# Performance work log

Hardware: AMD Instinct MI355X
Metric: run time of the kernel (lower is better)

Reference implementation:

```python
import jax, jax.numpy as jnp
import numpy as np

D_MODEL = 1024
N_HEADS = 16
HEAD_DIM = D_MODEL // N_HEADS
WINDOW = 256


def setup_inputs() -> dict:
    key = jax.random.key(0)
    kx, kq, ko = jax.random.split(key, 3)
    B, T = 4, 2048
    x = jax.random.normal(kx, (B, T, D_MODEL), dtype=jnp.float32)
    s = 1.0 / np.sqrt(D_MODEL)
    w_qkv = jax.random.normal(kq, (D_MODEL, 3 * D_MODEL), dtype=jnp.float32) * s
    w_out = jax.random.normal(ko, (D_MODEL, D_MODEL), dtype=jnp.float32) * s
    return {"x": x, "w_qkv": w_qkv, "w_out": w_out}


def reference(x, w_qkv, w_out):
    B, T, C = x.shape
    qkv = (x @ w_qkv).reshape(B, T, 3, N_HEADS, HEAD_DIM)
    q, k, v = qkv[:, :, 0], qkv[:, :, 1], qkv[:, :, 2]  # [B,T,H,D]
    # sliding-window causal mask: position i attends to j in (i-W, i]
    i = jnp.arange(T)[:, None]
    j = jnp.arange(T)[None, :]
    allowed = (j <= i) & (j > i - WINDOW)
    mask = jnp.where(allowed, 0.0, -jnp.inf).astype(x.dtype)  # [T,T]
    scale = 1.0 / np.sqrt(HEAD_DIM)
    scores = jnp.einsum('bqhd,bkhd->bhqk', q, k) * scale + mask
    attn = jax.nn.softmax(scores, axis=-1)
    out = jnp.einsum('bhqk,bkhd->bqhd', attn, v).reshape(B, T, C)
    return out @ w_out
```

## Files before the change

### kernel.cpp

```cpp
#include <hip/hip_runtime.h>

typedef unsigned short u16;
typedef __attribute__((ext_vector_type(8))) short bh8;
typedef __attribute__((ext_vector_type(4))) float f4;
typedef __attribute__((ext_vector_type(4))) unsigned short us4;

#define T_SEQ 2048
#define NHEADS 16
#define DHEAD 64
#define WIN 256

__device__ __forceinline__ float bf2f(u16 u) {
  union { unsigned int i; float f; } v; v.i = ((unsigned int)u) << 16; return v.f;
}
__device__ __forceinline__ u16 f2bf(float f) {
  unsigned int u = __float_as_uint(f);
  u = u + 0x7fffu + ((u >> 16) & 1u);
  return (u16)(u >> 16);
}
__device__ __forceinline__ void async16(const void* g, void* l) {
  void* gv = const_cast<void*>(g);
  __builtin_amdgcn_global_load_lds(
      (__attribute__((address_space(1))) void*)gv,
      (__attribute__((address_space(3))) void*)l, 16, 0, 0);
}

__device__ __forceinline__ int is_f32_probe(const void* x) {
  const float* xf = (const float*)x;
  const int lane = threadIdx.x & 63;
  int bad = 0;
  #pragma unroll
  for (int u = 0; u < 4; ++u) {
    const float v = xf[lane * 4 + u];
    const float a = fabsf(v);
    bad |= (!(a < 64.f)) || (!(v == 0.f || a > 1e-30f));
  }
  return __any(bad) ? 0 : 1;
}

__global__ __launch_bounds__(256) void prep(
    const void* __restrict__ x, const void* __restrict__ w_qkv,
    const void* __restrict__ w_out, u16* __restrict__ xbf,
    u16* __restrict__ wqkvT, u16* __restrict__ woutT, int have_x)
{
  const int bid = blockIdx.x;
  const int tid = threadIdx.x;
  const int isf = is_f32_probe(x);

  if (bid < 4096) {
    if (!have_x) return;
    const size_t e = ((size_t)bid * 256 + tid) * 8;
    if (isf) {
      const float* f = (const float*)x;
      us4 o0, o1;
      #pragma unroll
      for (int u = 0; u < 4; ++u) { o0[u] = f2bf(f[e + u]); o1[u] = f2bf(f[e + 4 + u]); }
      *(us4*)&xbf[e] = o0; *(us4*)&xbf[e + 4] = o1;
    } else {
      *(us4*)&xbf[e]     = *(const us4*)&((const u16*)x)[e];
      *(us4*)&xbf[e + 4] = *(const us4*)&((const u16*)x)[e + 4];
    }
  } else {
    __shared__ alignas(16) u16 tile[32][33];
    const void* in; u16* out; int C, bx, by;
    if (bid < 4096 + 3072) { const int t = bid - 4096; in = w_qkv; out = wqkvT; C = 3072; bx = t % 96; by = t / 96; }
    else                   { const int t = bid - 7168; in = w_out; out = woutT; C = 1024; bx = t % 32; by = t / 32; }
    const int R = 1024;
    const int tx = tid & 31, ty = tid >> 5;
    const int xg = bx * 32 + tx;
    const int y0 = by * 32;
    #pragma unroll
    for (int i = ty; i < 32; i += 8) {
      u16 v;
      if (isf) v = f2bf(((const float*)in)[(size_t)(y0 + i) * C + xg]);
      else     v = ((const u16*)in)[(size_t)(y0 + i) * C + xg];
      tile[i][tx] = v;
    }
    __syncthreads();
    const int ox  = y0 + tx;
    const int oy0 = bx * 32;
    #pragma unroll
    for (int i = ty; i < 32; i += 8)
      out[(size_t)(oy0 + i) * R + ox] = tile[tx][i];
  }
}

template<bool ADYN, bool CDYN>
__global__ __launch_bounds__(256, 4) void gemm_bt(
    const void* __restrict__ A, const u16* __restrict__ Bt,
    void* __restrict__ C, int N, int K, int lda, int ldc,
    const void* __restrict__ xprobe)
{
  __shared__ alignas(16) u16 As[128 * 64];
  __shared__ alignas(16) u16 Bs[128 * 64];

  const int isf  = (ADYN || CDYN) ? is_f32_probe(xprobe) : 0;
  const int tid  = threadIdx.x;
  const int lane = tid & 63;
  const int w    = tid >> 6;
  const int wm   = (w >> 1) * 64;
  const int wn   = (w & 1) * 64;
  const int quad = lane >> 4;
  const int l16  = lane & 15;
  const int row0 = blockIdx.y * 128;
  const int col0 = blockIdx.x * 128;

  f4 acc[4][4] = {};

  size_t aoff[4]; const u16* bsrc[4]; int lofs[4];
  #pragma unroll
  for (int s = 0; s < 4; ++s) {
    const int r  = s * 32 + (tid >> 3);
    const int gc = (tid & 7) ^ (r & 7);
    aoff[s] = (size_t)(row0 + r) * lda + gc * 8;
    bsrc[s] = Bt + (size_t)(col0 + r) * K + gc * 8;
    lofs[s] = s * 4096 + tid * 16;
  }

  const bool af32 = ADYN && isf;

  for (int k0 = 0; k0 < K; k0 += 64) {
    if (af32) {
      const float* Af = (const float*)A;
      bh8 a[4];
      #pragma unroll
      for (int s = 0; s < 4; ++s) {
        f4 u0 = *(const f4*)(Af + aoff[s] + k0);
        f4 u1 = *(const f4*)(Af + aoff[s] + k0 + 4);
        #pragma unroll
        for (int u = 0; u < 4; ++u) { a[s][u] = (short)f2bf(u0[u]); a[s][u + 4] = (short)f2bf(u1[u]); }
      }
      __syncthreads();
      #pragma unroll
      for (int s = 0; s < 4; ++s) {
        *(bh8*)((char*)As + lofs[s]) = a[s];
        async16(bsrc[s] + k0, (char*)Bs + lofs[s]);
      }
    } else {
      const u16* A16 = (const u16*)A;
      __syncthreads();
      #pragma unroll
      for (int s = 0; s < 4; ++s) {
        async16(A16 + aoff[s] + k0, (char*)As + lofs[s]);
        async16(bsrc[s] + k0,       (char*)Bs + lofs[s]);
      }
    }
    __builtin_amdgcn_s_waitcnt(0);
    __syncthreads();

    #pragma unroll
    for (int ks = 0; ks < 2; ++ks) {
      bh8 af[4], bf[4];
      #pragma unroll
      for (int i = 0; i < 4; ++i) {
        const int row = wm + i * 16 + l16;
        const int lc  = (ks * 4 + quad) ^ (row & 7);
        af[i] = *(const bh8*)(As + row * 64 + lc * 8);
      }
      #pragma unroll
      for (int j = 0; j < 4; ++j) {
        const int row = wn + j * 16 + l16;
        const int lc  = (ks * 4 + quad) ^ (row & 7);
        bf[j] = *(const bh8*)(Bs + row * 64 + lc * 8);
      }
      #pragma unroll
      for (int i = 0; i < 4; ++i)
        #pragma unroll
        for (int j = 0; j < 4; ++j)
          acc[i][j] = __builtin_amdgcn_mfma_f32_16x16x32_bf16(af[i], bf[j], acc[i][j], 0, 0, 0);
    }
  }

  const bool cf32 = CDYN && isf;
  #pragma unroll
  for (int i = 0; i < 4; ++i) {
    #pragma unroll
    for (int j = 0; j < 4; ++j) {
      const int rb = row0 + wm + i * 16 + quad * 4;
      const int cc = col0 + wn + j * 16 + l16;
      #pragma unroll
      for (int r = 0; r < 4; ++r) {
        if (cf32) ((float*)C)[(size_t)(rb + r) * ldc + cc] = acc[i][j][r];
        else      ((u16*)C)[(size_t)(rb + r) * ldc + cc]   = f2bf(acc[i][j][r]);
      }
    }
  }
}

__global__ __launch_bounds__(256) void attn_mfma(const u16* __restrict__ qkv,
                                                 u16* __restrict__ att, int ldo)
{
  __shared__ alignas(16) u16 Kt[64 * 72];
  __shared__ alignas(16) u16 Vt[64 * 72];
  __shared__ alignas(16) u16 Ps[64 * 72];

  const int tid  = threadIdx.x;
  const int lane = tid & 63;
  const int w    = tid >> 6;
  const int quad = lane >> 4;
  const int l16  = lane & 15;
  const int qb = blockIdx.x, h = blockIdx.y, b = blockIdx.z;
  const int qs = qb * 64;

  const u16* base = qkv + (size_t)b * T_SEQ * 3072 + h * 64;

  const size_t qrowg = (size_t)(qs + w * 16 + l16) * 3072;
  bh8 qa0 = *(const bh8*)&base[qrowg + quad * 8];
  bh8 qa1 = *(const bh8*)&base[qrowg + 32 + quad * 8];
  #pragma unroll
  for (int u = 0; u < 8; ++u) {
    qa0[u] = (short)f2bf(bf2f((u16)qa0[u]) * 0.125f);
    qa1[u] = (short)f2bf(bf2f((u16)qa1[u]) * 0.125f);
  }

  f4 Oc[4] = {};
  float mst[4] = {-1e30f, -1e30f, -1e30f, -1e30f};
  float lst[4] = {0.f, 0.f, 0.f, 0.f};

  const int tmin = (qb >= 4) ? 0 : (4 - qb);
  const int c8  = (tid & 7) * 8;
  const int r0s = tid >> 3;

  for (int t = tmin; t < 5; ++t) {
    const int kt0 = qs - 256 + t * 64;
    const bool diag  = (t == 4);
    const bool ledge = (t == 0);
    const int kb_lo = ledge ? w : 0;
    const int kb_hi = diag  ? w : 3;
    __syncthreads();

    #pragma unroll
    for (int r = r0s; r < 64; r += 32) {
      *(bh8*)&Kt[r * 72 + c8] =
          *(const bh8*)&base[(size_t)(kt0 + r) * 3072 + 1024 + c8];
      bh8 v = *(const bh8*)&base[(size_t)(kt0 + r) * 3072 + 2048 + c8];
      const int kc = r >> 3, ki = r & 7;
      #pragma unroll
      for (int u = 0; u < 8; ++u) {
        const int d = c8 + u;
        Vt[d * 72 + ((kc ^ (d >> 3)) << 3) + ki] = (u16)v[u];
      }
    }
    __syncthreads();

    f4 S[4];
    #pragma unroll
    for (int kb = 0; kb < 4; ++kb) {
      if (kb < kb_lo || kb > kb_hi) {
        S[kb][0] = S[kb][1] = S[kb][2] = S[kb][3] = -1e30f;
      } else {
        const int krow = (kb * 16 + l16) * 72;
        bh8 kf0 = *(const bh8*)&Kt[krow + quad * 8];
        bh8 kf1 = *(const bh8*)&Kt[krow + 32 + quad * 8];
        f4 s = {};
        s = __builtin_amdgcn_mfma_f32_16x16x32_bf16(qa0, kf0, s, 0, 0, 0);
        s = __builtin_amdgcn_mfma_f32_16x16x32_bf16(qa1, kf1, s, 0, 0, 0);
        S[kb] = s;
      }
    }

    if (diag || ledge) {
      #pragma unroll
      for (int kb = 0; kb < 4; ++kb) {
        if (kb == w) {
          #pragma unroll
          for (int rr = 0; rr < 4; ++rr) {
            const int ii = quad * 4 + rr;
            const bool ok = diag ? (l16 <= ii) : (l16 > ii);
            if (!ok) S[kb][rr] = -1e30f;
          }
        }
      }
    }

    float tmax[4] = {-1e30f, -1e30f, -1e30f, -1e30f};
    #pragma unroll
    for (int kb = 0; kb < 4; ++kb)
      #pragma unroll
      for (int rr = 0; rr < 4; ++rr)
        tmax[rr] = fmaxf(tmax[rr], S[kb][rr]);
    #pragma unroll
    for (int off = 1; off < 16; off <<= 1)
      #pragma unroll
      for (int rr = 0; rr < 4; ++rr)
        tmax[rr] = fmaxf(tmax[rr], __shfl_xor(tmax[rr], off));

    const bool grew = (tmax[0] > mst[0] + 8.f) || (tmax[1] > mst[1] + 8.f) ||
                      (tmax[2] > mst[2] + 8.f) || (tmax[3] > mst[3] + 8.f);
    if (__any(grew)) {
      #pragma unroll
      for (int rr = 0; rr < 4; ++rr) {
        const float mnew = fmaxf(mst[rr], tmax[rr]);
        const float al = __expf(mst[rr] - mnew);
        mst[rr] = mnew;
        lst[rr] *= al;
        #pragma unroll
        for (int db = 0; db < 4; ++db) Oc[db][rr] *= al;
      }
    }

    float rsum[4] = {0.f, 0.f, 0.f, 0.f};
    const int swq = quad >> 1;
    #pragma unroll
    for (int kb = 0; kb < 4; ++kb) {
      const int kc = kb * 2 + (l16 >> 3);
      const int ki = l16 & 7;
      #pragma unroll
      for (int rr = 0; rr < 4; ++rr) {
        const float p = __expf(S[kb][rr] - mst[rr]);
        rsum[rr] += p;
        const int q = w * 16 + quad * 4 + rr;
        Ps[q * 72 + ((kc ^ swq) << 3) + ki] = f2bf(p);
      }
    }
    #pragma unroll
    for (int off = 1; off < 16; off <<= 1)
      #pragma unroll
      for (int rr = 0; rr < 4; ++rr)
        rsum[rr] += __shfl_xor(rsum[rr], off);
    #pragma unroll
    for (int rr = 0; rr < 4; ++rr)
      lst[rr] += rsum[rr];

    {
      const int q = w * 16 + l16;
      const int sw = (q >> 3) & 1;
      bh8 pa0 = *(const bh8*)&Ps[q * 72 + (((0 + quad) ^ sw) << 3)];
      bh8 pa1 = *(const bh8*)&Ps[q * 72 + (((4 + quad) ^ sw) << 3)];
      #pragma unroll
      for (int db = 0; db < 4; ++db) {
        const int d = db * 16 + l16;
        const int dsw = d >> 3;
        bh8 vb0 = *(const bh8*)&Vt[d * 72 + (((0 + quad) ^ dsw) << 3)];
        bh8 vb1 = *(const bh8*)&Vt[d * 72 + (((4 + quad) ^ dsw) << 3)];
        Oc[db] = __builtin_amdgcn_mfma_f32_16x16x32_bf16(pa0, vb0, Oc[db], 0, 0, 0);
        Oc[db] = __builtin_amdgcn_mfma_f32_16x16x32_bf16(pa1, vb1, Oc[db], 0, 0, 0);
      }
    }
  }

  u16* obase = att + (size_t)b * T_SEQ * ldo + h * 64;
  #pragma unroll
  for (int rr = 0; rr < 4; ++rr) {
    const int i = qs + w * 16 + quad * 4 + rr;
    const float inv = 1.f / lst[rr];
    #pragma unroll
    for (int db = 0; db < 4; ++db)
      obase[(size_t)i * ldo + db * 16 + l16] = f2bf(Oc[db][rr] * inv);
  }
}

extern "C" void kernel_launch(void* const* d_in, const int* in_sizes, int n_in,
                              void* d_out, int out_size, void* d_ws, size_t ws_size,
                              hipStream_t stream) {
  const void* x     = d_in[0];
  const void* w_qkv = d_in[1];
  const void* w_out = d_in[2];

  const size_t SZ_QKV = (size_t)8192 * 3072 * 2;
  const size_t SZ_XBF = (size_t)8192 * 1024 * 2;
  const size_t SZ_WQ  = (size_t)3072 * 1024 * 2;
  const size_t SZ_WO  = (size_t)1024 * 1024 * 2;
  const size_t SZ_ATT = (size_t)8192 * 1024 * 2;

  char* p = (char*)d_ws;
  u16* qkv   = (u16*)p; p += SZ_QKV;
  u16* wqkvT = (u16*)p; p += SZ_WQ;
  u16* woutT = (u16*)p; p += SZ_WO;
  u16* xbf   = (u16*)p; p += SZ_XBF;
  u16* attb  = (u16*)p;
  const size_t need_x   = SZ_QKV + SZ_WQ + SZ_WO + SZ_XBF;
  const bool have_x   = ws_size >= need_x;
  const bool have_att = ws_size >= need_x + SZ_ATT;

  prep<<<dim3(8192), 256, 0, stream>>>(x, w_qkv, w_out, xbf, wqkvT, woutT,
                                       have_x ? 1 : 0);

  if (have_x) {
    gemm_bt<false, false><<<dim3(24, 64), 256, 0, stream>>>(
        xbf, wqkvT, qkv, 3072, 1024, 1024, 3072, x);
  } else {
    gemm_bt<true, false><<<dim3(24, 64), 256, 0, stream>>>(
        x, wqkvT, qkv, 3072, 1024, 1024, 3072, x);
  }

  u16* attp  = have_att ? attb : qkv;
  const int ldo = have_att ? 1024 : 3072;
  attn_mfma<<<dim3(32, NHEADS, 4), 256, 0, stream>>>(qkv, attp, ldo);

  gemm_bt<false, true><<<dim3(8, 64), 256, 0, stream>>>(
      attp, woutT, d_out, 1024, 1024, ldo, 1024, x);
}
```

Before: 226.6 us.

## Add double-buffered 256x128 GEMM and pre-transposed V attention path

Adds a new 512-thread GEMM kernel with 256x128 tiles, double-buffered async global-to-LDS loads, split B-fragment phases and s_setprio around the MFMA bursts. It is used for both the QKV and output projections. Adds a separate V-transpose kernel so the attention kernel can fill K and V into swizzled LDS with async loads instead of per-element scattered transposes. This removes load latency and LDS scatter cost, but adds one extra kernel launch and an extra round trip of V through memory, and it needs more workspace.

After: 234.6 us. 1.04x slower.

```diff
diff --git a/kernel.cpp b/kernel.cpp
--- a/kernel.cpp
+++ b/kernel.cpp
@@ -9,6 +9,9 @@
 #define NHEADS 16
 #define DHEAD 64
 #define WIN 256
+
+#define MF(a, b, c) __builtin_amdgcn_mfma_f32_16x16x32_bf16((a), (b), (c), 0, 0, 0)
+#define VMCNT(n) asm volatile("s_waitcnt vmcnt(" #n ")" ::: "memory")
 
 __device__ __forceinline__ float bf2f(u16 u) {
   union { unsigned int i; float f; } v; v.i = ((unsigned int)u) << 16; return v.f;
@@ -167,7 +170,7 @@
       for (int i = 0; i < 4; ++i)
         #pragma unroll
         for (int j = 0; j < 4; ++j)
-          acc[i][j] = __builtin_amdgcn_mfma_f32_16x16x32_bf16(af[i], bf[j], acc[i][j], 0, 0, 0);
+          acc[i][j] = MF(af[i], bf[j], acc[i][j]);
     }
   }
 
@@ -187,11 +190,155 @@
   }
 }
 
-__global__ __launch_bounds__(256) void attn_mfma(const u16* __restrict__ qkv,
-                                                 u16* __restrict__ att, int ldo)
+template<bool CDYN>
+__global__ __launch_bounds__(512, 2) void gemm2(
+    const u16* __restrict__ A, const u16* __restrict__ Bt, void* __restrict__ C,
+    int K, int lda, int ldc, const void* __restrict__ xprobe)
 {
-  __shared__ alignas(16) u16 Kt[64 * 72];
-  __shared__ alignas(16) u16 Vt[64 * 72];
+  __shared__ alignas(16) u16 As[2 * 256 * 64];
+  __shared__ alignas(16) u16 Bs[2 * 128 * 64];
+
+  const int isf  = CDYN ? is_f32_probe(xprobe) : 0;
+  const int tid  = threadIdx.x;
+  const int lane = tid & 63;
+  const int w    = tid >> 6;
+  const int wm   = (w >> 1) * 64;
+  const int wn   = (w & 1) * 64;
+  const int quad = lane >> 4;
+  const int l16  = lane & 15;
+  const int row0 = blockIdx.y * 256;
+  const int col0 = blockIdx.x * 128;
+
+  f4 acc[4][4] = {};
+
+  const int rs = tid >> 3;
+  const int cs = tid & 7;
+  const u16* apt[4]; const u16* bpt[2];
+  #pragma unroll
+  for (int s = 0; s < 4; ++s) {
+    const int r = s * 64 + rs;
+    apt[s] = A + (size_t)(row0 + r) * lda + (cs ^ (r & 7)) * 8;
+  }
+  #pragma unroll
+  for (int s = 0; s < 2; ++s) {
+    const int r = s * 64 + rs;
+    bpt[s] = Bt + (size_t)(col0 + r) * K + (cs ^ (r & 7)) * 8;
+  }
+  const int soff = tid * 16;
+  const int NK = K >> 6;
+
+#define STAGE_A2(buf, kk) do { \
+    async16(apt[0] + (kk), (char*)As + (buf) * 32768 +     0 + soff); \
+    async16(apt[1] + (kk), (char*)As + (buf) * 32768 +  8192 + soff); \
+    async16(apt[2] + (kk), (char*)As + (buf) * 32768 + 16384 + soff); \
+    async16(apt[3] + (kk), (char*)As + (buf) * 32768 + 24576 + soff); } while (0)
+#define STAGE_B2(buf, kk) do { \
+    async16(bpt[0] + (kk), (char*)Bs + (buf) * 16384 +     0 + soff); \
+    async16(bpt[1] + (kk), (char*)Bs + (buf) * 16384 +  8192 + soff); } while (0)
+
+  const int sw = l16 & 7;
+  const int c0 = (quad ^ sw) * 8;
+  const int c1 = ((quad + 4) ^ sw) * 8;
+  int ra[4], rb[4];
+  #pragma unroll
+  for (int i = 0; i < 4; ++i) ra[i] = (wm + i * 16 + l16) * 64;
+  #pragma unroll
+  for (int j = 0; j < 4; ++j) rb[j] = (wn + j * 16 + l16) * 64;
+
+  STAGE_A2(0, 0); STAGE_B2(0, 0);
+  if (NK > 1) { STAGE_A2(1, 64); STAGE_B2(1, 64); VMCNT(6); }
+  else        { VMCNT(0); }
+  __builtin_amdgcn_s_barrier();
+
+  for (int T = 0; T < NK; ++T) {
+    const u16* Ab = As + (T & 1) * 16384;
+    const u16* Bb = Bs + (T & 1) * 8192;
+
+    bh8 a[4][2], b0[2][2];
+    #pragma unroll
+    for (int i = 0; i < 4; ++i) {
+      a[i][0] = *(const bh8*)(Ab + ra[i] + c0);
+      a[i][1] = *(const bh8*)(Ab + ra[i] + c1);
+    }
+    #pragma unroll
+    for (int j = 0; j < 2; ++j) {
+      b0[j][0] = *(const bh8*)(Bb + rb[j] + c0);
+      b0[j][1] = *(const bh8*)(Bb + rb[j] + c1);
+    }
+    if (T >= 1 && T + 1 < NK) STAGE_B2((T + 1) & 1, (T + 1) * 64);
+    __builtin_amdgcn_s_barrier();
+    __builtin_amdgcn_s_setprio(1);
+    #pragma unroll
+    for (int i = 0; i < 4; ++i)
+      #pragma unroll
+      for (int j = 0; j < 2; ++j)
+        acc[i][j] = MF(a[i][1], b0[j][1], MF(a[i][0], b0[j][0], acc[i][j]));
+    __builtin_amdgcn_s_setprio(0);
+    __builtin_amdgcn_s_barrier();
+
+    bh8 b1[2][2];
+    #pragma unroll
+    for (int j = 0; j < 2; ++j) {
+      b1[j][0] = *(const bh8*)(Bb + rb[2 + j] + c0);
+      b1[j][1] = *(const bh8*)(Bb + rb[2 + j] + c1);
+    }
+    if (T + 2 < NK) STAGE_A2(T & 1, (T + 2) * 64);
+    __builtin_amdgcn_s_barrier();
+    __builtin_amdgcn_s_setprio(1);
+    #pragma unroll
+    for (int i = 0; i < 4; ++i)
+      #pragma unroll
+      for (int j = 0; j < 2; ++j)
+        acc[i][2 + j] = MF(a[i][1], b1[j][1], MF(a[i][0], b1[j][0], acc[i][2 + j]));
+    __builtin_amdgcn_s_setprio(0);
+    if (T + 2 < NK) { VMCNT(4); } else { VMCNT(0); }
+    __builtin_amdgcn_s_barrier();
+  }
+#undef STAGE_A2
+#undef STAGE_B2
+
+  const bool cf32 = CDYN && isf;
+  #pragma unroll
+  for (int i = 0; i < 4; ++i) {
+    #pragma unroll
+    for (int j = 0; j < 4; ++j) {
+      const int rr0 = row0 + wm + i * 16 + quad * 4;
+      const int cc  = col0 + wn + j * 16 + l16;
+      #pragma unroll
+      for (int r = 0; r < 4; ++r) {
+        if (cf32) ((float*)C)[(size_t)(rr0 + r) * ldc + cc] = acc[i][j][r];
+        else      ((u16*)C)[(size_t)(rr0 + r) * ldc + cc]   = f2bf(acc[i][j][r]);
+      }
+    }
+  }
+}
+
+__global__ __launch_bounds__(256) void vtrans(const u16* __restrict__ qkv,
+                                              u16* __restrict__ vT)
+{
+  __shared__ alignas(16) u16 tile[32][33];
+  const int tid = threadIdx.x;
+  const int bh = blockIdx.z;
+  const int b = bh >> 4, h = bh & 15;
+  const int k0 = blockIdx.x * 32, d0 = blockIdx.y * 32;
+  const int tx = tid & 31, ty = tid >> 5;
+  const u16* src = qkv + (size_t)b * T_SEQ * 3072 + 2048 + h * 64;
+  #pragma unroll
+  for (int i = ty; i < 32; i += 8)
+    tile[i][tx] = src[(size_t)(k0 + i) * 3072 + d0 + tx];
+  __syncthreads();
+  u16* dst = vT + ((size_t)bh * 64 + d0) * T_SEQ + k0;
+  #pragma unroll
+  for (int i = ty; i < 32; i += 8)
+    dst[(size_t)i * T_SEQ + tx] = tile[tx][i];
+}
+
+__global__ __launch_bounds__(256) void attn_mfma2(const u16* __restrict__ qkv,
+                                                  const u16* __restrict__ vT,
+                                                  u16* __restrict__ att, int ldo)
+{
+  __shared__ alignas(16) u16 Kt[64 * 64];
+  __shared__ alignas(16) u16 Vt[64 * 64];
   __shared__ alignas(16) u16 Ps[64 * 72];
 
   const int tid  = threadIdx.x;
@@ -203,6 +350,7 @@
   const int qs = qb * 64;
 
   const u16* base = qkv + (size_t)b * T_SEQ * 3072 + h * 64;
+  const u16* vTbh = vT + (size_t)(b * NHEADS + h) * 64 * T_SEQ;
 
   const size_t qrowg = (size_t)(qs + w * 16 + l16) * 3072;
   bh8 qa0 = *(const bh8*)&base[qrowg + quad * 8];
@@ -218,8 +366,10 @@
   float lst[4] = {0.f, 0.f, 0.f, 0.f};
 
   const int tmin = (qb >= 4) ? 0 : (4 - qb);
-  const int c8  = (tid & 7) * 8;
-  const int r0s = tid >> 3;
+  const int srow0 = tid >> 3;
+  const int srow1 = 32 + (tid >> 3);
+  const int gc0 = (tid & 7) ^ (srow0 & 7);
+  const int gc1 = (tid & 7) ^ (srow1 & 7);
 
   for (int t = tmin; t < 5; ++t) {
     const int kt0 = qs - 256 + t * 64;
@@ -227,37 +377,32 @@
     const bool ledge = (t == 0);
     const int kb_lo = ledge ? w : 0;
     const int kb_hi = diag  ? w : 3;
+
     __syncthreads();
-
-    #pragma unroll
-    for (int r = r0s; r < 64; r += 32) {
-      *(bh8*)&Kt[r * 72 + c8] =
-          *(const bh8*)&base[(size_t)(kt0 + r) * 3072 + 1024 + c8];
-      bh8 v = *(const bh8*)&base[(size_t)(kt0 + r) * 3072 + 2048 + c8];
-      const int kc = r >> 3, ki = r & 7;
-      #pragma unroll
-      for (int u = 0; u < 8; ++u) {
-        const int d = c8 + u;
-        Vt[d * 72 + ((kc ^ (d >> 3)) << 3) + ki] = (u16)v[u];
-      }
-    }
+    async16(&base[(size_t)(kt0 + srow0) * 3072 + 1024 + gc0 * 8], (char*)Kt + tid * 16);
+    async16(&base[(size_t)(kt0 + srow1) * 3072 + 1024 + gc1 * 8], (char*)Kt + 4096 + tid * 16);
+    async16(vTbh + (size_t)srow0 * T_SEQ + kt0 + gc0 * 8, (char*)Vt + tid * 16);
+    async16(vTbh + (size_t)srow1 * T_SEQ + kt0 + gc1 * 8, (char*)Vt + 4096 + tid * 16);
+    __builtin_amdgcn_s_waitcnt(0);
     __syncthreads();
 
     f4 S[4];
+    __builtin_amdgcn_s_setprio(1);
     #pragma unroll
     for (int kb = 0; kb < 4; ++kb) {
       if (kb < kb_lo || kb > kb_hi) {
         S[kb][0] = S[kb][1] = S[kb][2] = S[kb][3] = -1e30f;
       } else {
-        const int krow = (kb * 16 + l16) * 72;
-        bh8 kf0 = *(const bh8*)&Kt[krow + quad * 8];
-        bh8 kf1 = *(const bh8*)&Kt[krow + 32 + quad * 8];
+        const int row = kb * 16 + l16;
+        bh8 kf0 = *(const bh8*)&Kt[row * 64 + ((quad    ) ^ (row & 7)) * 8];
+        bh8 kf1 = *(const bh8*)&Kt[row * 64 + ((quad + 4) ^ (row & 7)) * 8];
         f4 s = {};
-        s = __builtin_amdgcn_mfma_f32_16x16x32_bf16(qa0, kf0, s, 0, 0, 0);
-        s = __builtin_amdgcn_mfma_f32_16x16x32_bf16(qa1, kf1, s, 0, 0, 0);
+        s = MF(qa0, kf0, s);
+        s = MF(qa1, kf1, s);
         S[kb] = s;
       }
     }
+    __builtin_amdgcn_s_setprio(0);
 
     if (diag || ledge) {
       #pragma unroll
@@ -324,17 +469,181 @@
 
     {
       const int q = w * 16 + l16;
-      const int sw = (q >> 3) & 1;
-      bh8 pa0 = *(const bh8*)&Ps[q * 72 + (((0 + quad) ^ sw) << 3)];
-      bh8 pa1 = *(const bh8*)&Ps[q * 72 + (((4 + quad) ^ sw) << 3)];
+      const int swp = (q >> 3) & 1;
+      bh8 pa0 = *(const bh8*)&Ps[q * 72 + (((0 + quad) ^ swp) << 3)];
+      bh8 pa1 = *(const bh8*)&Ps[q * 72 + (((4 + quad) ^ swp) << 3)];
+      __builtin_amdgcn_s_setprio(1);
+      #pragma unroll
+      for (int db = 0; db < 4; ++db) {
+        const int d = db * 16 + l16;
+        bh8 vb0 = *(const bh8*)&Vt[d * 64 + ((quad    ) ^ (d & 7)) * 8];
+        bh8 vb1 = *(const bh8*)&Vt[d * 64 + ((quad + 4) ^ (d & 7)) * 8];
+        Oc[db] = MF(pa0, vb0, Oc[db]);
+        Oc[db] = MF(pa1, vb1, Oc[db]);
+      }
+      __builtin_amdgcn_s_setprio(0);
+    }
+  }
+
+  u16* obase = att + (size_t)b * T_SEQ * ldo + h * 64;
+  #pragma unroll
+  for (int rr = 0; rr < 4; ++rr) {
+    const int i = qs + w * 16 + quad * 4 + rr;
+    const float inv = 1.f / lst[rr];
+    #pragma unroll
+    for (int db = 0; db < 4; ++db)
+      obase[(size_t)i * ldo + db * 16 + l16] = f2bf(Oc[db][rr] * inv);
+  }
+}
+
+__global__ __launch_bounds__(256) void attn_mfma(const u16* __restrict__ qkv,
+                                                 u16* __restrict__ att, int ldo)
+{
+  __shared__ alignas(16) u16 Kt[64 * 72];
+  __shared__ alignas(16) u16 Vt[64 * 72];
+  __shared__ alignas(16) u16 Ps[64 * 72];
+
+  const int tid  = threadIdx.x;
+  const int lane = tid & 63;
+  const int w    = tid >> 6;
+  const int quad = lane >> 4;
+  const int l16  = lane & 15;
+  const int qb = blockIdx.x, h = blockIdx.y, b = blockIdx.z;
+  const int qs = qb * 64;
+
+  const u16* base = qkv + (size_t)b * T_SEQ * 3072 + h * 64;
+
+  const size_t qrowg = (size_t)(qs + w * 16 + l16) * 3072;
+  bh8 qa0 = *(const bh8*)&base[qrowg + quad * 8];
+  bh8 qa1 = *(const bh8*)&base[qrowg + 32 + quad * 8];
+  #pragma unroll
+  for (int u = 0; u < 8; ++u) {
+    qa0[u] = (short)f2bf(bf2f((u16)qa0[u]) * 0.125f);
+    qa1[u] = (short)f2bf(bf2f((u16)qa1[u]) * 0.125f);
+  }
+
+  f4 Oc[4] = {};
+  float mst[4] = {-1e30f, -1e30f, -1e30f, -1e30f};
+  float lst[4] = {0.f, 0.f, 0.f, 0.f};
+
+  const int tmin = (qb >= 4) ? 0 : (4 - qb);
+  const int c8  = (tid & 7) * 8;
+  const int r0s = tid >> 3;
+
+  for (int t = tmin; t < 5; ++t) {
+    const int kt0 = qs - 256 + t * 64;
+    const bool diag  = (t == 4);
+    const bool ledge = (t == 0);
+    const int kb_lo = ledge ? w : 0;
+    const int kb_hi = diag  ? w : 3;
+    __syncthreads();
+
+    #pragma unroll
+    for (int r = r0s; r < 64; r += 32) {
+      *(bh8*)&Kt[r * 72 + c8] =
+          *(const bh8*)&base[(size_t)(kt0 + r) * 3072 + 1024 + c8];
+      bh8 v = *(const bh8*)&base[(size_t)(kt0 + r) * 3072 + 2048 + c8];
+      const int kc = r >> 3, ki = r & 7;
+      #pragma unroll
+      for (int u = 0; u < 8; ++u) {
+        const int d = c8 + u;
+        Vt[d * 72 + ((kc ^ (d >> 3)) << 3) + ki] = (u16)v[u];
+      }
+    }
+    __syncthreads();
+
+    f4 S[4];
+    #pragma unroll
+    for (int kb = 0; kb < 4; ++kb) {
+      if (kb < kb_lo || kb > kb_hi) {
+        S[kb][0] = S[kb][1] = S[kb][2] = S[kb][3] = -1e30f;
+      } else {
+        const int krow = (kb * 16 + l16) * 72;
+        bh8 kf0 = *(const bh8*)&Kt[krow + quad * 8];
+        bh8 kf1 = *(const bh8*)&Kt[krow + 32 + quad * 8];
+        f4 s = {};
+        s = MF(qa0, kf0, s);
+        s = MF(qa1, kf1, s);
+        S[kb] = s;
+      }
+    }
+
+    if (diag || ledge) {
+      #pragma unroll
+      for (int kb = 0; kb < 4; ++kb) {
+        if (kb == w) {
+          #pragma unroll
+          for (int rr = 0; rr < 4; ++rr) {
+            const int ii = quad * 4 + rr;
+            const bool ok = diag ? (l16 <= ii) : (l16 > ii);
+            if (!ok) S[kb][rr] = -1e30f;
+          }
+        }
+      }
+    }
+
+    float tmax[4] = {-1e30f, -1e30f, -1e30f, -1e30f};
+    #pragma unroll
+    for (int kb = 0; kb < 4; ++kb)
+      #pragma unroll
+      for (int rr = 0; rr < 4; ++rr)
+        tmax[rr] = fmaxf(tmax[rr], S[kb][rr]);
+    #pragma unroll
+    for (int off = 1; off < 16; off <<= 1)
+      #pragma unroll
+      for (int rr = 0; rr < 4; ++rr)
+        tmax[rr] = fmaxf(tmax[rr], __shfl_xor(tmax[rr], off));
+
+    const bool grew = (tmax[0] > mst[0] + 8.f) || (tmax[1] > mst[1] + 8.f) ||
+                      (tmax[2] > mst[2] + 8.f) || (tmax[3] > mst[3] + 8.f);
+    if (__any(grew)) {
+      #pragma unroll
+      for (int rr = 0; rr < 4; ++rr) {
+        const float mnew = fmaxf(mst[rr], tmax[rr]);
+        const float al = __expf(mst[rr] - mnew);
+        mst[rr] = mnew;
+        lst[rr] *= al;
+        #pragma unroll
+        for (int db = 0; db < 4; ++db) Oc[db][rr] *= al;
+      }
+    }
+
+    float rsum[4] = {0.f, 0.f, 0.f, 0.f};
+    const int swq = quad >> 1;
+    #pragma unroll
+    for (int kb = 0; kb < 4; ++kb) {
+      const int kc = kb * 2 + (l16 >> 3);
+      const int ki = l16 & 7;
+      #pragma unroll
+      for (int rr = 0; rr < 4; ++rr) {
+        const float p = __expf(S[kb][rr] - mst[rr]);
+        rsum[rr] += p;
+        const int q = w * 16 + quad * 4 + rr;
+        Ps[q * 72 + ((kc ^ swq) << 3) + ki] = f2bf(p);
+      }
+    }
+    #pragma unroll
+    for (int off = 1; off < 16; off <<= 1)
+      #pragma unroll
+      for (int rr = 0; rr < 4; ++rr)
+        rsum[rr] += __shfl_xor(rsum[rr], off);
+    #pragma unroll
+    for (int rr = 0; rr < 4; ++rr)
+      lst[rr] += rsum[rr];
+
+    {
+      const int q = w * 16 + l16;
+      const int swp = (q >> 3) & 1;
+      bh8 pa0 = *(const bh8*)&Ps[q * 72 + (((0 + quad) ^ swp) << 3)];
+      bh8 pa1 = *(const bh8*)&Ps[q * 72 + (((4 + quad) ^ swp) << 3)];
       #pragma unroll
       for (int db = 0; db < 4; ++db) {
         const int d = db * 16 + l16;
         const int dsw = d >> 3;
         bh8 vb0 = *(const bh8*)&Vt[d * 72 + (((0 + quad) ^ dsw) << 3)];
         bh8 vb1 = *(const bh8*)&Vt[d * 72 + (((4 + quad) ^ dsw) << 3)];
-        Oc[db] = __builtin_amdgcn_mfma_f32_16x16x32_bf16(pa0, vb0, Oc[db], 0, 0, 0);
-        Oc[db] = __builtin_amdgcn_mfma_f32_16x16x32_bf16(pa1, vb1, Oc[db], 0, 0, 0);
+        Oc[db] = MF(pa0, vb0, Oc[db]);
+        Oc[db] = MF(pa1, vb1, Oc[db]);
       }
     }
   }
@@ -361,6 +670,7 @@
   const size_t SZ_XBF = (size_t)8192 * 1024 * 2;
   const size_t SZ_WQ  = (size_t)3072 * 1024 * 2;
   const size_t SZ_WO  = (size_t)1024 * 1024 * 2;
+  const size_t SZ_VT  = (size_t)64 * 64 * 2048 * 2;
   const size_t SZ_ATT = (size_t)8192 * 1024 * 2;
 
   char* p = (char*)d_ws;
@@ -368,26 +678,38 @@
   u16* wqkvT = (u16*)p; p += SZ_WQ;
   u16* woutT = (u16*)p; p += SZ_WO;
   u16* xbf   = (u16*)p; p += SZ_XBF;
+  u16* vTb   = (u16*)p; p += SZ_VT;
   u16* attb  = (u16*)p;
-  const size_t need_x   = SZ_QKV + SZ_WQ + SZ_WO + SZ_XBF;
-  const bool have_x   = ws_size >= need_x;
-  const bool have_att = ws_size >= need_x + SZ_ATT;
+  const size_t need_x  = SZ_QKV + SZ_WQ + SZ_WO + SZ_XBF;
+  const bool have_x    = ws_size >= need_x;
+  const bool have_vt   = ws_size >= need_x + SZ_VT;
+  const bool have_att  = ws_size >= need_x + SZ_VT + SZ_ATT;
 
   prep<<<dim3(8192), 256, 0, stream>>>(x, w_qkv, w_out, xbf, wqkvT, woutT,
                                        have_x ? 1 : 0);
 
   if (have_x) {
-    gemm_bt<false, false><<<dim3(24, 64), 256, 0, stream>>>(
-        xbf, wqkvT, qkv, 3072, 1024, 1024, 3072, x);
+    gemm2<false><<<dim3(24, 32), 512, 0, stream>>>(
+        xbf, wqkvT, qkv, 1024, 1024, 3072, x);
   } else {
     gemm_bt<true, false><<<dim3(24, 64), 256, 0, stream>>>(
         x, wqkvT, qkv, 3072, 1024, 1024, 3072, x);
   }
 
-  u16* attp  = have_att ? attb : qkv;
+  u16* attp = have_att ? attb : qkv;
   const int ldo = have_att ? 1024 : 3072;
-  attn_mfma<<<dim3(32, NHEADS, 4), 256, 0, stream>>>(qkv, attp, ldo);
-
-  gemm_bt<false, true><<<dim3(8, 64), 256, 0, stream>>>(
-      attp, woutT, d_out, 1024, 1024, ldo, 1024, x);
-}
+  if (have_vt) {
+    vtrans<<<dim3(64, 2, 64), 256, 0, stream>>>(qkv, vTb);
+    attn_mfma2<<<dim3(32, NHEADS, 4), 256, 0, stream>>>(qkv, vTb, attp, ldo);
+  } else {
+    attn_mfma<<<dim3(32, NHEADS, 4), 256, 0, stream>>>(qkv, attp, ldo);
+  }
+
+  if (have_x) {
+    gemm2<true><<<dim3(8, 32), 512, 0, stream>>>(
+        attp, woutT, d_out, 1024, ldo, 1024, x);
+  } else {
+    gemm_bt<false, true><<<dim3(8, 64), 256, 0, stream>>>(
+        attp, woutT, d_out, 1024, 1024, ldo, 1024, x);
+  }
+}
```

## Rewrite windowed attention as single-pass block with full K/V window in LDS

Applied to the files above, without the earlier changes.

The attention kernel now processes 128 query rows per 512-thread block and loads the whole 384-row K/V window into LDS once, K through async global-to-LDS copies. Scores for all 17 key tiles stay in registers, and softmax runs without max subtraction or online rescaling. This removes the per-tile sync loop and repeated K/V reloads. Separately, the GEMM gets an XCD-aware block swizzle and the weight transpose in prep is vectorised. Skipping the max subtraction risks exp overflow if scores get large, and the larger LDS footprint and register use may lower occupancy.

Measured after the change: 224.5 us. About the same (-0.9%).

```diff
diff --git a/kernel.cpp b/kernel.cpp
--- a/kernel.cpp
+++ b/kernel.cpp
@@ -4,11 +4,14 @@
 typedef __attribute__((ext_vector_type(8))) short bh8;
 typedef __attribute__((ext_vector_type(4))) float f4;
 typedef __attribute__((ext_vector_type(4))) unsigned short us4;
+typedef __attribute__((ext_vector_type(8))) unsigned short us8;
 
 #define T_SEQ 2048
 #define NHEADS 16
 #define DHEAD 64
 #define WIN 256
+
+#define MF(a, b, c) __builtin_amdgcn_mfma_f32_16x16x32_bf16((a), (b), (c), 0, 0, 0)
 
 __device__ __forceinline__ float bf2f(u16 u) {
   union { unsigned int i; float f; } v; v.i = ((unsigned int)u) << 16; return v.f;
@@ -66,22 +69,24 @@
     if (bid < 4096 + 3072) { const int t = bid - 4096; in = w_qkv; out = wqkvT; C = 3072; bx = t % 96; by = t / 96; }
     else                   { const int t = bid - 7168; in = w_out; out = woutT; C = 1024; bx = t % 32; by = t / 32; }
     const int R = 1024;
-    const int tx = tid & 31, ty = tid >> 5;
-    const int xg = bx * 32 + tx;
+    const int tx4 = (tid & 7) * 4;
+    const int iy  = tid >> 3;
     const int y0 = by * 32;
-    #pragma unroll
-    for (int i = ty; i < 32; i += 8) {
-      u16 v;
-      if (isf) v = f2bf(((const float*)in)[(size_t)(y0 + i) * C + xg]);
-      else     v = ((const u16*)in)[(size_t)(y0 + i) * C + xg];
-      tile[i][tx] = v;
+    if (isf) {
+      f4 v = *(const f4*)&((const float*)in)[(size_t)(y0 + iy) * C + bx * 32 + tx4];
+      #pragma unroll
+      for (int u = 0; u < 4; ++u) tile[iy][tx4 + u] = f2bf(v[u]);
+    } else {
+      us4 v = *(const us4*)&((const u16*)in)[(size_t)(y0 + iy) * C + bx * 32 + tx4];
+      #pragma unroll
+      for (int u = 0; u < 4; ++u) tile[iy][tx4 + u] = v[u];
     }
     __syncthreads();
-    const int ox  = y0 + tx;
-    const int oy0 = bx * 32;
-    #pragma unroll
-    for (int i = ty; i < 32; i += 8)
-      out[(size_t)(oy0 + i) * R + ox] = tile[tx][i];
+    const int i2 = tid >> 3;
+    us4 o;
+    #pragma unroll
+    for (int u = 0; u < 4; ++u) o[u] = tile[tx4 + u][i2];
+    *(us4*)&out[(size_t)(bx * 32 + i2) * R + y0 + tx4] = o;
   }
 }
 
@@ -102,8 +107,18 @@
   const int wn   = (w & 1) * 64;
   const int quad = lane >> 4;
   const int l16  = lane & 15;
-  const int row0 = blockIdx.y * 128;
-  const int col0 = blockIdx.x * 128;
+
+  int bx = blockIdx.x, by = blockIdx.y;
+  {
+    const int nx = gridDim.x, nwg = nx * gridDim.y;
+    if ((nwg & 7) == 0) {
+      const int lin = by * nx + bx;
+      const int sw  = (lin & 7) * (nwg >> 3) + (lin >> 3);
+      bx = sw % nx; by = sw / nx;
+    }
+  }
+  const int row0 = by * 128;
+  const int col0 = bx * 128;
 
   f4 acc[4][4] = {};
 
@@ -167,7 +182,7 @@
       for (int i = 0; i < 4; ++i)
         #pragma unroll
         for (int j = 0; j < 4; ++j)
-          acc[i][j] = __builtin_amdgcn_mfma_f32_16x16x32_bf16(af[i], bf[j], acc[i][j], 0, 0, 0);
+          acc[i][j] = MF(af[i], bf[j], acc[i][j]);
     }
   }
 
@@ -187,12 +202,12 @@
   }
 }
 
-__global__ __launch_bounds__(256) void attn_mfma(const u16* __restrict__ qkv,
-                                                 u16* __restrict__ att, int ldo)
+__global__ __launch_bounds__(512) void attn_win(const u16* __restrict__ qkv,
+                                                u16* __restrict__ att, int ldo)
 {
-  __shared__ alignas(16) u16 Kt[64 * 72];
-  __shared__ alignas(16) u16 Vt[64 * 72];
-  __shared__ alignas(16) u16 Ps[64 * 72];
+  __shared__ alignas(16) u16 Kt[384 * 64];
+  __shared__ alignas(16) u16 Vt[64 * 384];
+  __shared__ alignas(16) u16 Ps[8 * 16 * 72];
 
   const int tid  = threadIdx.x;
   const int lane = tid & 63;
@@ -200,11 +215,36 @@
   const int quad = lane >> 4;
   const int l16  = lane & 15;
   const int qb = blockIdx.x, h = blockIdx.y, b = blockIdx.z;
-  const int qs = qb * 64;
+  const int qs = qb * 128;
+  const int kbase = qs - 256;
 
   const u16* base = qkv + (size_t)b * T_SEQ * 3072 + h * 64;
 
-  const size_t qrowg = (size_t)(qs + w * 16 + l16) * 3072;
+  #pragma unroll
+  for (int s = 0; s < 6; ++s) {
+    const int id = s * 512 + tid;
+    const int r  = id >> 3;
+    const int gc = (id & 7) ^ (r & 7);
+    int gk = kbase + r; gk = gk < 0 ? 0 : gk;
+    async16(&base[(size_t)gk * 3072 + 1024 + gc * 8], (char*)Kt + id * 16);
+  }
+  #pragma unroll
+  for (int s = 0; s < 6; ++s) {
+    const int id = s * 512 + tid;
+    const int r  = id >> 3;
+    const int dc = id & 7;
+    int gk = kbase + r; gk = gk < 0 ? 0 : gk;
+    us8 v = *(const us8*)&base[(size_t)gk * 3072 + 2048 + dc * 8];
+    const int g = r >> 3, j = r & 7;
+    #pragma unroll
+    for (int u = 0; u < 8; ++u) {
+      const int d = dc * 8 + u;
+      Vt[d * 384 + ((g ^ (d & 7)) << 3) + j] = v[u];
+    }
+  }
+
+  const int q0w = qs + w * 16;
+  const size_t qrowg = (size_t)(q0w + l16) * 3072;
   bh8 qa0 = *(const bh8*)&base[qrowg + quad * 8];
   bh8 qa1 = *(const bh8*)&base[qrowg + 32 + quad * 8];
   #pragma unroll
@@ -213,137 +253,95 @@
     qa1[u] = (short)f2bf(bf2f((u16)qa1[u]) * 0.125f);
   }
 
+  __builtin_amdgcn_s_waitcnt(0);
+  __syncthreads();
+
+  const int qw16 = (qs >> 4) + w;
+  const int t_lo = qw16 >= 16 ? 0 : 16 - qw16;
+  const bool has_ledge = (t_lo == 0);
+
+  f4 S[17];
+  __builtin_amdgcn_s_setprio(1);
+  #pragma unroll
+  for (int t = 0; t < 17; ++t) {
+    if (t >= t_lo) {
+      const int kr = 16 * (w + t) + l16;
+      const int sw = l16 & 7;
+      bh8 kf0 = *(const bh8*)&Kt[kr * 64 + ((quad    ) ^ sw) * 8];
+      bh8 kf1 = *(const bh8*)&Kt[kr * 64 + ((quad + 4) ^ sw) * 8];
+      f4 s = {};
+      s = MF(qa0, kf0, s);
+      s = MF(qa1, kf1, s);
+      S[t] = s;
+    }
+  }
+  __builtin_amdgcn_s_setprio(0);
+
+  #pragma unroll
+  for (int rr = 0; rr < 4; ++rr) {
+    const int ii = quad * 4 + rr;
+    if (l16 > ii) S[16][rr] = -1e30f;
+    if (has_ledge && l16 <= ii) S[0][rr] = -1e30f;
+  }
+
+  float rsum[4] = {0.f, 0.f, 0.f, 0.f};
+  #pragma unroll
+  for (int t = 0; t < 17; ++t) {
+    if (t >= t_lo) {
+      #pragma unroll
+      for (int rr = 0; rr < 4; ++rr) {
+        const float p = __expf(S[t][rr]);
+        S[t][rr] = p;
+        rsum[rr] += p;
+      }
+    }
+  }
+  #pragma unroll
+  for (int off = 1; off < 16; off <<= 1)
+    #pragma unroll
+    for (int rr = 0; rr < 4; ++rr)
+      rsum[rr] += __shfl_xor(rsum[rr], off);
+
+  u16* Psw = Ps + w * 16 * 72;
   f4 Oc[4] = {};
-  float mst[4] = {-1e30f, -1e30f, -1e30f, -1e30f};
-  float lst[4] = {0.f, 0.f, 0.f, 0.f};
-
-  const int tmin = (qb >= 4) ? 0 : (4 - qb);
-  const int c8  = (tid & 7) * 8;
-  const int r0s = tid >> 3;
-
-  for (int t = tmin; t < 5; ++t) {
-    const int kt0 = qs - 256 + t * 64;
-    const bool diag  = (t == 4);
-    const bool ledge = (t == 0);
-    const int kb_lo = ledge ? w : 0;
-    const int kb_hi = diag  ? w : 3;
-    __syncthreads();
-
-    #pragma unroll
-    for (int r = r0s; r < 64; r += 32) {
-      *(bh8*)&Kt[r * 72 + c8] =
-          *(const bh8*)&base[(size_t)(kt0 + r) * 3072 + 1024 + c8];
-      bh8 v = *(const bh8*)&base[(size_t)(kt0 + r) * 3072 + 2048 + c8];
-      const int kc = r >> 3, ki = r & 7;
-      #pragma unroll
-      for (int u = 0; u < 8; ++u) {
-        const int d = c8 + u;
-        Vt[d * 72 + ((kc ^ (d >> 3)) << 3) + ki] = (u16)v[u];
-      }
-    }
-    __syncthreads();
-
-    f4 S[4];
+  const int swq = quad >> 1;
+  const int swp = (l16 >> 3) & 1;
+  #pragma unroll
+  for (int g = 0; g < 5; ++g) {
+    if (4 * g + 3 < t_lo && g != 4) continue;
     #pragma unroll
     for (int kb = 0; kb < 4; ++kb) {
-      if (kb < kb_lo || kb > kb_hi) {
-        S[kb][0] = S[kb][1] = S[kb][2] = S[kb][3] = -1e30f;
-      } else {
-        const int krow = (kb * 16 + l16) * 72;
-        bh8 kf0 = *(const bh8*)&Kt[krow + quad * 8];
-        bh8 kf1 = *(const bh8*)&Kt[krow + 32 + quad * 8];
-        f4 s = {};
-        s = __builtin_amdgcn_mfma_f32_16x16x32_bf16(qa0, kf0, s, 0, 0, 0);
-        s = __builtin_amdgcn_mfma_f32_16x16x32_bf16(qa1, kf1, s, 0, 0, 0);
-        S[kb] = s;
-      }
-    }
-
-    if (diag || ledge) {
-      #pragma unroll
-      for (int kb = 0; kb < 4; ++kb) {
-        if (kb == w) {
-          #pragma unroll
-          for (int rr = 0; rr < 4; ++rr) {
-            const int ii = quad * 4 + rr;
-            const bool ok = diag ? (l16 <= ii) : (l16 > ii);
-            if (!ok) S[kb][rr] = -1e30f;
-          }
-        }
-      }
-    }
-
-    float tmax[4] = {-1e30f, -1e30f, -1e30f, -1e30f};
-    #pragma unroll
-    for (int kb = 0; kb < 4; ++kb)
-      #pragma unroll
-      for (int rr = 0; rr < 4; ++rr)
-        tmax[rr] = fmaxf(tmax[rr], S[kb][rr]);
-    #pragma unroll
-    for (int off = 1; off < 16; off <<= 1)
-      #pragma unroll
-      for (int rr = 0; rr < 4; ++rr)
-        tmax[rr] = fmaxf(tmax[rr], __shfl_xor(tmax[rr], off));
-
-    const bool grew = (tmax[0] > mst[0] + 8.f) || (tmax[1] > mst[1] + 8.f) ||
-                      (tmax[2] > mst[2] + 8.f) || (tmax[3] > mst[3] + 8.f);
-    if (__any(grew)) {
-      #pragma unroll
-      for (int rr = 0; rr < 4; ++rr) {
-        const float mnew = fmaxf(mst[rr], tmax[rr]);
-        const float al = __expf(mst[rr] - mnew);
-        mst[rr] = mnew;
-        lst[rr] *= al;
-        #pragma unroll
-        for (int db = 0; db < 4; ++db) Oc[db][rr] *= al;
-      }
-    }
-
-    float rsum[4] = {0.f, 0.f, 0.f, 0.f};
-    const int swq = quad >> 1;
-    #pragma unroll
-    for (int kb = 0; kb < 4; ++kb) {
+      const int t = 4 * g + kb;
       const int kc = kb * 2 + (l16 >> 3);
       const int ki = l16 & 7;
       #pragma unroll
       for (int rr = 0; rr < 4; ++rr) {
-        const float p = __expf(S[kb][rr] - mst[rr]);
-        rsum[rr] += p;
-        const int q = w * 16 + quad * 4 + rr;
-        Ps[q * 72 + ((kc ^ swq) << 3) + ki] = f2bf(p);
-      }
-    }
-    #pragma unroll
-    for (int off = 1; off < 16; off <<= 1)
-      #pragma unroll
-      for (int rr = 0; rr < 4; ++rr)
-        rsum[rr] += __shfl_xor(rsum[rr], off);
-    #pragma unroll
-    for (int rr = 0; rr < 4; ++rr)
-      lst[rr] += rsum[rr];
-
-    {
-      const int q = w * 16 + l16;
-      const int sw = (q >> 3) & 1;
-      bh8 pa0 = *(const bh8*)&Ps[q * 72 + (((0 + quad) ^ sw) << 3)];
-      bh8 pa1 = *(const bh8*)&Ps[q * 72 + (((4 + quad) ^ sw) << 3)];
-      #pragma unroll
-      for (int db = 0; db < 4; ++db) {
-        const int d = db * 16 + l16;
-        const int dsw = d >> 3;
-        bh8 vb0 = *(const bh8*)&Vt[d * 72 + (((0 + quad) ^ dsw) << 3)];
-        bh8 vb1 = *(const bh8*)&Vt[d * 72 + (((4 + quad) ^ dsw) << 3)];
-        Oc[db] = __builtin_amdgcn_mfma_f32_16x16x32_bf16(pa0, vb0, Oc[db], 0, 0, 0);
-        Oc[db] = __builtin_amdgcn_mfma_f32_16x16x32_bf16(pa1, vb1, Oc[db], 0, 0, 0);
-      }
-    }
+        const int qloc = quad * 4 + rr;
+        const u16 pv = (t <= 16 && t >= t_lo) ? f2bf(S[t][rr]) : (u16)0;
+        Psw[qloc * 72 + ((kc ^ swq) << 3) + ki] = pv;
+      }
+    }
+    bh8 pa0 = *(const bh8*)&Psw[l16 * 72 + (((0 + quad) ^ swp) << 3)];
+    bh8 pa1 = *(const bh8*)&Psw[l16 * 72 + (((4 + quad) ^ swp) << 3)];
+    __builtin_amdgcn_s_setprio(1);
+    #pragma unroll
+    for (int db = 0; db < 4; ++db) {
+      const int d = db * 16 + l16;
+      int cc0 = 2 * w + 8 * g + quad;     cc0 = cc0 > 47 ? 47 : cc0;
+      int cc1 = 2 * w + 8 * g + quad + 4; cc1 = cc1 > 47 ? 47 : cc1;
+      bh8 vb0 = *(const bh8*)&Vt[d * 384 + (cc0 ^ (d & 7)) * 8];
+      bh8 vb1 = *(const bh8*)&Vt[d * 384 + (cc1 ^ (d & 7)) * 8];
+      Oc[db] = MF(pa0, vb0, Oc[db]);
+      Oc[db] = MF(pa1, vb1, Oc[db]);
+    }
+    __builtin_amdgcn_s_setprio(0);
   }
 
   u16* obase = att + (size_t)b * T_SEQ * ldo + h * 64;
   #pragma unroll
   for (int rr = 0; rr < 4; ++rr) {
-    const int i = qs + w * 16 + quad * 4 + rr;
-    const float inv = 1.f / lst[rr];
+    const int i = q0w + quad * 4 + rr;
+    const float inv = 1.f / rsum[rr];
     #pragma unroll
     for (int db = 0; db < 4; ++db)
       obase[(size_t)i * ldo + db * 16 + l16] = f2bf(Oc[db][rr] * inv);
@@ -369,9 +367,9 @@
   u16* woutT = (u16*)p; p += SZ_WO;
   u16* xbf   = (u16*)p; p += SZ_XBF;
   u16* attb  = (u16*)p;
-  const size_t need_x   = SZ_QKV + SZ_WQ + SZ_WO + SZ_XBF;
-  const bool have_x   = ws_size >= need_x;
-  const bool have_att = ws_size >= need_x + SZ_ATT;
+  const size_t need_x  = SZ_QKV + SZ_WQ + SZ_WO + SZ_XBF;
+  const bool have_x    = ws_size >= need_x;
+  const bool have_att  = ws_size >= need_x + SZ_ATT;
 
   prep<<<dim3(8192), 256, 0, stream>>>(x, w_qkv, w_out, xbf, wqkvT, woutT,
                                        have_x ? 1 : 0);
@@ -384,9 +382,9 @@
         x, wqkvT, qkv, 3072, 1024, 1024, 3072, x);
   }
 
-  u16* attp  = have_att ? attb : qkv;
+  u16* attp = have_att ? attb : qkv;
   const int ldo = have_att ? 1024 : 3072;
-  attn_mfma<<<dim3(32, NHEADS, 4), 256, 0, stream>>>(qkv, attp, ldo);
+  attn_win<<<dim3(16, NHEADS, 4), 512, 0, stream>>>(qkv, attp, ldo);
 
   gemm_bt<false, true><<<dim3(8, 64), 256, 0, stream>>>(
       attp, woutT, d_out, 1024, 1024, ldo, 1024, x);
```
